# Optimization experiments

Hardware: AMD Instinct MI355X
Metric: run time of the kernel (lower is better)

## Reference

```python
import jax, jax.numpy as jnp
import numpy as np

P1, P2, M1, M2, W_SEARCH, STEP = 7, 7, 18, 55, 37, 4
EPS = 1e-6  # F.pairwise_distance eps


def align_corners(x, s, value):
    N, C, H, W = x.shape
    i = (s - H % s + 1) % s
    j = (s - W % s + 1) % s
    x = jnp.pad(x, ((0, 0), (0, 0), (0, i), (0, j)), constant_values=value)
    rows = jnp.array([H - 1, H - 1 + i]); cols = jnp.arange(0, W - 1, s)
    sub = x[:, :, rows[:, None], cols[None, :]]
    x = x.at[:, :, rows[:, None], cols[None, :]].set(sub[:, :, ::-1, :])
    rws = jnp.arange(0, H - 1, s); cls = jnp.array([W - 1, W - 1 + j])
    sub = x[:, :, rws[:, None], cls[None, :]]
    x = x.at[:, :, rws[:, None], cls[None, :]].set(sub[:, :, :, ::-1])
    rr = jnp.array([H - 1, H - 1 + i]); cc = jnp.array([W - 1, W - 1 + j])
    sub = x[:, :, rr, cc]
    x = x.at[:, :, rr, cc].set(sub[:, :, ::-1])
    return x


def unfold(x, p):  # torch F.unfold ordering: (N, C*p*p, (H-p+1)*(W-p+1))
    N, C, H, W = x.shape
    Hp, Wp = H - p + 1, W - p + 1
    cols = jnp.stack([x[:, :, ki:ki + Hp, kj:kj + Wp] for ki in range(p) for kj in range(p)], axis=2)
    return cols.reshape(N, C * p * p, Hp * Wp)


def fold(cols, H, W, p, C):  # torch F.fold: overlap-add
    N = cols.shape[0]; Hp, Wp = H - p + 1, W - p + 1
    cols = cols.reshape(N, C, p, p, Hp, Wp)
    out = jnp.zeros((N, C, H, W), cols.dtype)
    for ki in range(p):
        for kj in range(p):
            out = out.at[:, :, ki:ki + Hp, kj:kj + Wp].add(cols[:, :, ki, kj])
    return out


def block_matching(x, m, p, w, s):
    v = w // 2
    N, C, H, W = x.shape
    patches = unfold(x, p).reshape(N, C * p * p, H - p + 1, W - p + 1)
    patches = align_corners(patches, s, jnp.inf)
    _, d, k, l = patches.shape
    ref = patches[:, :, ::s, ::s].transpose(0, 2, 3, 1)                # (N,K,L,d)
    pad = jnp.pad(patches, ((0, 0), (0, 0), (v, v), (v, v)), constant_values=jnp.inf).transpose(0, 2, 3, 1)
    K, L = ref.shape[1], ref.shape[2]
    col_idx = jnp.arange(w)[:, None] + s * jnp.arange(L)[None, :]      # (w,L)
    dists = []
    for i in range(w):  # fixed-size search-window loop (hyperparameter)
        pad_i = pad[:, i:i + k:s, :, :]                                # (N,K,l+2v,d)
        g = pad_i[:, :, col_idx, :]                                    # (N,K,w,L,d)
        diff = g - ref[:, :, None, :, :] + EPS
        dists.append(jnp.sqrt(jnp.sum(diff * diff, axis=-1)))         # (N,K,w,L)
    dist = jnp.stack(dists, axis=2)                                    # (N,K,wi,wj,L)
    dist = dist.transpose(0, 1, 4, 2, 3).reshape(N, K, L, w * w)
    dist = dist.at[:, :, :, v * w + v].set(-jnp.inf)                   # force self-match
    idx = jax.lax.top_k(-dist, m)[1]                                   # (N,K,L,m) smallest distances
    ind_row = idx // w - v
    ind_col = idx % w - v
    row_ref = align_corners(jnp.arange(H - p + 1).reshape(1, 1, -1, 1), s, 0)[0, 0, ::s, 0]
    col_ref = align_corners(jnp.arange(W - p + 1).reshape(1, 1, 1, -1), s, 0)[0, 0, 0, ::s]
    ir = jnp.minimum(row_ref[None, :, None, None] + ind_row, H - p)
    ic = jnp.minimum(col_ref[None, None, :, None] + ind_col, W - p)
    return (ir * (W - p + 1) + ic).reshape(N, -1)                      # (N, K*L*m), block-major then m


def group_patches(y, indices, m, p):
    N, C, H, W = y.shape
    n = C * p * p
    unf = unfold(y, p)
    g = jnp.take_along_axis(unf, jnp.broadcast_to(indices[:, None, :], (N, n, indices.shape[1])), axis=2)
    return g.transpose(0, 2, 1).reshape(N, -1, m, n)                   # (N,B,m,n)


def denoise1(Y, sigma):
    N, B, m, n = Y.shape
    YtY = jnp.einsum('nbik,nbjk->nbij', Y, Y)
    Lc = jnp.linalg.cholesky(YtY)
    rhs = YtY - n * sigma ** 2 * jnp.eye(m, dtype=Y.dtype)
    theta = jax.scipy.linalg.cho_solve((Lc, True), rhs)
    X_hat = jnp.einsum('nbij,nbjk->nbik', theta, Y)
    wts = 1.0 / jnp.clip(jnp.sum(theta ** 2, axis=3, keepdims=True), 1.0 / m, 1.0)
    return X_hat, wts


def denoise2(Y, X, sigma):
    N, B, m, n = Y.shape
    XtX = jnp.einsum('nbik,nbjk->nbij', X, X)
    Lc = jnp.linalg.cholesky(XtX + n * sigma ** 2 * jnp.eye(m, dtype=Y.dtype))
    theta = jax.scipy.linalg.cho_solve((Lc, True), XtX)
    X_hat = jnp.einsum('nbij,nbjk->nbik', theta, Y)
    wts = 1.0 / jnp.clip(jnp.sum(theta ** 2, axis=3, keepdims=True), 1.0 / m, 1.0)
    return X_hat, wts


def aggregation(X_hat, wts, indices, size, p):
    N, C, H, W = size
    n = C * p * p
    Ltot = (H - p + 1) * (W - p + 1)
    Xc = (X_hat * wts).transpose(0, 3, 1, 2).reshape(N, n, -1)         # (N,n,B*m)
    wc = jnp.broadcast_to(wts.reshape(N, 1, -1), Xc.shape)

    def scat(cols, idx):
        return jnp.zeros((n, Ltot), cols.dtype).at[:, idx].add(cols)

    Xs = jax.vmap(scat)(Xc, indices)
    Ws = jax.vmap(scat)(wc, indices)
    return fold(Xs, H, W, p, C) / fold(Ws, H, W, p, C)


def nlridge(input_y, sigma):
    # step 1: noisy self-similarity + ridge with known sigma
    y_mean = jnp.mean(input_y, axis=1, keepdims=True)
    idx1 = block_matching(jax.lax.stop_gradient(y_mean), M1, P1, W_SEARCH, STEP)
    Y1 = group_patches(input_y, idx1, M1, P1)
    X1, w1 = denoise1(Y1, sigma)
    den1 = aggregation(X1, w1, idx1, input_y.shape, P1)
    # step 2: pilot-guided matching + ridge
    x_mean = jnp.mean(den1, axis=1, keepdims=True)
    idx2 = block_matching(jax.lax.stop_gradient(x_mean), M2, P2, W_SEARCH, STEP)
    Y2 = group_patches(input_y, idx2, M2, P2)
    X2 = group_patches(den1, idx2, M2, P2)
    Xh, w2 = denoise2(Y2, X2, sigma)
    return aggregation(Xh, w2, idx2, input_y.shape, P2)


def setup_inputs() -> dict:
    key = jax.random.key(0)
    input_y = jax.random.uniform(key, (2, 1, 256, 256), dtype=jnp.float32)
    sigma = jnp.array([0.1], dtype=jnp.float32)  # ~25/255 noise level
    return {'input_y': input_y, 'sigma': sigma}


def reference(input_y, sigma):
    return nlridge(input_y, sigma)
```

## Files before the change

### kernel.cpp

```cpp
#include <hip/hip_runtime.h>
#include <math.h>

#define IMG_H 256
#define IMG_W 256
#define IMG_SZ (IMG_H * IMG_W)
#define NP 49
#define HP 250
#define NPAT 62500
#define NB 4096
#define NCAND 1369
#define VRAD 18
#define CENTER (VRAD * 37 + VRAD)
#define NIMG 2
#define YSTR 52
#define WSTR 55

__device__ __forceinline__ bool align_map(int r, int c, int& ro, int& co) {
    if (r < 0 || r > 252 || c < 0 || c > 252) return false;
    if (r == 252) {
        if (c == 252) { ro = 249; co = 249; return true; }
        if (c <= 248 && (c & 3) == 0) { ro = 249; co = c; return true; }
        return false;
    }
    if (c == 252) {
        if (r <= 248 && (r & 3) == 0) { ro = r; co = 249; return true; }
        return false;
    }
    if (r >= 250 || c >= 250) return false;
    if (r == 249) {
        if (c == 249) return false;
        if ((c & 3) == 0) return false;
        ro = 249; co = c; return true;
    }
    if (c == 249) {
        if ((r & 3) == 0) return false;
        ro = r; co = 249; return true;
    }
    ro = r; co = c; return true;
}

__global__ void zero_kernel(float* __restrict__ p, int total) {
    int i = blockIdx.x * blockDim.x + threadIdx.x;
    if (i < total) p[i] = 0.0f;
}

__global__ void div_kernel(const float* __restrict__ acc, float* __restrict__ out, int total) {
    int i = blockIdx.x * blockDim.x + threadIdx.x;
    if (i < total) out[i] = acc[2 * i] / acc[2 * i + 1];
}

__global__ __launch_bounds__(256) void fold_div_kernel(const float* __restrict__ Xacc,
                                                       const float* __restrict__ Wacc,
                                                       float* __restrict__ out) {
    int e = blockIdx.x * 256 + threadIdx.x;
    if (e >= NIMG * IMG_SZ) return;
    int n = e / IMG_SZ, pix = e % IMG_SZ;
    int r = pix / IMG_W, c = pix % IMG_W;
    const float* Xn = Xacc + (size_t)n * NPAT * NP;
    const float* Wn = Wacc + (size_t)n * NPAT;
    float num = 0.f, den = 0.f;
#pragma unroll
    for (int ki = 0; ki < 7; ++ki) {
        int pr = r - ki;
        if (pr < 0 || pr > HP - 1) continue;
#pragma unroll
        for (int kj = 0; kj < 7; ++kj) {
            int pc = c - kj;
            if (pc < 0 || pc > HP - 1) continue;
            int p = pr * HP + pc;
            num += Xn[(size_t)p * NP + ki * 7 + kj];
            den += Wn[p];
        }
    }
    out[e] = num / den;
}

template <int M>
__global__ __launch_bounds__(256) void bm_kernel(const float* __restrict__ img,
                                                 int* __restrict__ idx_out) {
    __shared__ float win[43 * WSTR];
    __shared__ float dist[4][NCAND];
    const int llb = blockIdx.x, kk = blockIdx.y, n = blockIdx.z;
    const float* im = img + (size_t)n * IMG_SZ;
    const int t = threadIdx.x;
    const int w = t >> 6, lane = t & 63;
    const int ll = 4 * llb + w;
    const int rr = (kk < 63) ? 4 * kk : 249;
    const int cc = (ll < 63) ? 4 * ll : 249;
    const int ar0 = 4 * kk, ac0 = 4 * ll;
    const int acb = 16 * llb;
    const int row0 = max(0, ar0 - VRAD), col0 = max(0, acb - VRAD);
    const int row1 = min(IMG_H - 1, ar0 + VRAD + 6);
    const int col1 = min(IMG_W - 1, acb + 12 + VRAD + 6);
    const int nr = row1 - row0 + 1, nc = col1 - col0 + 1;
    for (int e = t; e < nr * nc; e += 256) {
        int r = e / nc, c = e % nc;
        win[r * WSTR + c] = im[(row0 + r) * IMG_W + col0 + c];
    }
    __syncthreads();
    float rf[NP];
    {
        const float* rb = &win[(rr - row0) * WSTR + (cc - col0)];
#pragma unroll
        for (int ki = 0; ki < 7; ++ki)
#pragma unroll
            for (int kj = 0; kj < 7; ++kj) rf[ki * 7 + kj] = rb[ki * WSTR + kj];
    }
    float* dw = dist[w];
    for (int cand = lane; cand < NCAND; cand += 64) {
        const int dr = cand / 37 - VRAD, dc = cand % 37 - VRAD;
        int ro, co;
        float d;
        if (align_map(ar0 + dr, ac0 + dc, ro, co)) {
            const float* base = &win[(ro - row0) * WSTR + (co - col0)];
            float s = 0.f;
#pragma unroll
            for (int ki = 0; ki < 7; ++ki)
#pragma unroll
                for (int kj = 0; kj < 7; ++kj) {
                    float df = base[ki * WSTR + kj] - rf[ki * 7 + kj] + 1e-6f;
                    s = fmaf(df, df, s);
                }
            d = sqrtf(s);
        } else {
            d = INFINITY;
        }
        if (cand == CENTER) d = -1.0f;
        dw[cand] = d;
    }
    __syncthreads();
    float v1 = INFINITY, v2 = INFINITY;
    int i1 = NCAND, i2 = NCAND;
    for (int c = lane; c < NCAND; c += 64) {
        float v = dw[c];
        if (v < v1) { v2 = v1; i2 = i1; v1 = v; i1 = c; }
        else if (v < v2) { v2 = v; i2 = c; }
    }
    int* out = idx_out + (size_t)((n * 64 + kk) * 64 + ll) * M;
    for (int sel = 0; sel < M; ++sel) {
        float gv = v1;
        int gi = i1;
#pragma unroll
        for (int off = 32; off; off >>= 1) {
            float vv = __shfl_xor(gv, off);
            int ii = __shfl_xor(gi, off);
            if (vv < gv || (vv == gv && ii < gi)) { gv = vv; gi = ii; }
        }
        if (lane == 0) {
            int dr = gi / 37 - VRAD, dc = gi % 37 - VRAD;
            out[sel] = min(rr + dr, 249) * HP + min(cc + dc, 249);
        }
        if ((gi & 63) == lane) {
            dw[gi] = INFINITY;
            v1 = v2; i1 = i2; v2 = INFINITY; i2 = NCAND;
            if (i1 == NCAND) {
                for (int c = lane; c < NCAND; c += 64) {
                    float v = dw[c];
                    if (v < v1) { v2 = v1; i2 = i1; v1 = v; i1 = c; }
                    else if (v < v2) { v2 = v; i2 = c; }
                }
            }
        }
    }
}

template <int M, bool R2, bool AGGP>
__global__ __launch_bounds__(128, 2) void denoise_kernel(
    const float* __restrict__ y, const float* __restrict__ xsrc,
    const int* __restrict__ idx, const float* __restrict__ sigma_p,
    float* __restrict__ accPix, float* __restrict__ Xacc, float* __restrict__ Wacc) {
    constexpr int PADM = (M + 3) & ~3;
    constexpr int NCH = PADM / 4;
    constexpr int TPK = M * (M + 1) / 2;
    constexpr int NS = (TPK + 127) / 128;
    struct RO { static constexpr int f(int i) {
        int a = i >> 2, b = i & 3; return 8 * a * (a + 1) + 4 * (a + 1) * b; } };
    constexpr int LSZ = RO::f(PADM);
    constexpr int YOFF = LSZ;
    constexpr int UN = LSZ + M * YSTR;
    __shared__ __align__(16) float SU[UN];
    __shared__ float cbuf[64];
    __shared__ __align__(16) float rdiag[PADM];
    __shared__ float wsh[M];
    __shared__ int gix[M];
    const int b = blockIdx.x, n = blockIdx.y;
    const int t = threadIdx.x;
    const int lane = t & 63, wv = t >> 6;
    if (t < M) gix[t] = idx[(size_t)(n * NB + b) * M + t];
    __syncthreads();
    const float* im = y + (size_t)n * IMG_SZ;
    const float* xim = xsrc + (size_t)n * IMG_SZ;
    {
        const float* src = R2 ? xim : im;
        float* dst = R2 ? &SU[0] : &SU[YOFF];
        for (int e = t; e < M * YSTR; e += 128) {
            int i = e / YSTR, ch = e - i * YSTR;
            float v = 0.f;
            if (ch < NP) {
                int p = gix[i];
                v = src[(p / HP + ch / 7) * IMG_W + (p % HP + ch % 7)];
            }
            dst[i * YSTR + ch] = v;
        }
    }
    __syncthreads();
    const float sg = sigma_p[0];
    const float cns = 49.f * sg * sg;
    int siR[NS], sjR[NS];
    float gsum[NS];
#pragma unroll
    for (int s = 0; s < NS; ++s) {
        int e = t + 128 * s;
        if (e < TPK) {
            int i = (int)((sqrtf(8.f * e + 1.f) - 1.f) * 0.5f);
            while ((i + 1) * (i + 2) / 2 <= e) ++i;
            while (i * (i + 1) / 2 > e) --i;
            siR[s] = i;
            sjR[s] = e - i * (i + 1) / 2;
        } else {
            siR[s] = -1;
            sjR[s] = 0;
        }
    }
    {
        const float* base = R2 ? &SU[0] : &SU[YOFF];
#pragma unroll
        for (int s = 0; s < NS; ++s) {
            float sum = 0.f;
            if (siR[s] >= 0) {
                const float* Pi = base + siR[s] * YSTR;
                const float* Pj = base + sjR[s] * YSTR;
#pragma unroll
                for (int q = 0; q < 13; ++q) {
                    float4 a = *(const float4*)(Pi + 4 * q);
                    float4 c4 = *(const float4*)(Pj + 4 * q);
                    sum = fmaf(a.x, c4.x, sum);
                    sum = fmaf(a.y, c4.y, sum);
                    sum = fmaf(a.z, c4.z, sum);
                    sum = fmaf(a.w, c4.w, sum);
                }
                if (R2 && siR[s] == sjR[s]) sum += cns;
            }
            gsum[s] = sum;
        }
    }
    __syncthreads();
#pragma unroll
    for (int s = 0; s < NS; ++s)
        if (siR[s] >= 0) SU[RO::f(siR[s]) + sjR[s]] = gsum[s];
    if (R2) {
        for (int e = t; e < M * YSTR; e += 128) {
            int i = e / YSTR, ch = e - i * YSTR;
            float v = 0.f;
            if (ch < NP) {
                int p = gix[i];
                v = im[(p / HP + ch / 7) * IMG_W + (p % HP + ch % 7)];
            }
            SU[YOFF + i * YSTR + ch] = v;
        }
    }
    __syncthreads();
    if (wv == 0) {
        float g[PADM];
        if (lane < M) {
#pragma unroll
            for (int j = 0; j < PADM; ++j) {
                if (j >= M) g[j] = 0.f;
                else g[j] = (j <= lane) ? SU[RO::f(lane) + j] : SU[RO::f(j) + lane];
            }
        } else {
#pragma unroll
            for (int j = 0; j < PADM; ++j) g[j] = (j == lane) ? 1.f : 0.f;
        }
#pragma unroll
        for (int k = 0; k < PADM - 1; ++k) {
            cbuf[lane] = g[k];
            float ivd = 1.f / cbuf[k];
            float fk = g[k] * ivd;
#pragma unroll
            for (int jb = (k + 1) / 4; jb < NCH; ++jb) {
                float4 cv = *(const float4*)&cbuf[4 * jb];
                if (4 * jb + 0 > k) g[4 * jb + 0] = fmaf(-fk, cv.x, g[4 * jb + 0]);
                if (4 * jb + 1 > k) g[4 * jb + 1] = fmaf(-fk, cv.y, g[4 * jb + 1]);
                if (4 * jb + 2 > k) g[4 * jb + 2] = fmaf(-fk, cv.z, g[4 * jb + 2]);
                if (4 * jb + 3 > k) g[4 * jb + 3] = fmaf(-fk, cv.w, g[4 * jb + 3]);
            }
        }
        if (lane < PADM) rdiag[lane] = (lane < M) ? 1.f / sqrtf(g[lane]) : 1.f;
        if (lane < PADM) {
#pragma unroll
            for (int jb = 0; jb < NCH; ++jb) {
                if (4 * jb <= lane) {
                    float4 rd4 = *(const float4*)&rdiag[4 * jb];
                    float4 o;
                    o.x = g[4 * jb + 0] * rd4.x;
                    o.y = g[4 * jb + 1] * rd4.y;
                    o.z = g[4 * jb + 2] * rd4.z;
                    o.w = g[4 * jb + 3] * rd4.w;
                    *(float4*)&SU[RO::f(lane) + 4 * jb] = o;
                }
            }
        }
    }
    __syncthreads();
    const bool isId = (wv == 0) && (lane < M);
    const bool isY = (wv == 1) && (lane < NP);
    const int ch = (wv == 1 && lane < NP) ? lane : 0;
    float bb[PADM];
    if (wv == 1) {
#pragma unroll
        for (int i = 0; i < PADM; ++i) bb[i] = (i < M) ? SU[YOFF + i * YSTR + ch] : 0.f;
    } else {
#pragma unroll
        for (int i = 0; i < PADM; ++i) bb[i] = (i == lane) ? 1.f : 0.f;
    }
#pragma unroll
    for (int ck = 0; ck < NCH; ++ck) {
        const int i0 = 4 * ck;
        float L10 = SU[RO::f(4 * ck + 1) + 4 * ck];
        float L20 = SU[RO::f(4 * ck + 2) + 4 * ck], L21 = SU[RO::f(4 * ck + 2) + 4 * ck + 1];
        float L30 = SU[RO::f(4 * ck + 3) + 4 * ck], L31 = SU[RO::f(4 * ck + 3) + 4 * ck + 1],
              L32 = SU[RO::f(4 * ck + 3) + 4 * ck + 2];
        float b0 = bb[i0] * rdiag[i0];
        float b1 = (bb[i0 + 1] - L10 * b0) * rdiag[i0 + 1];
        float b2 = (bb[i0 + 2] - L20 * b0 - L21 * b1) * rdiag[i0 + 2];
        float b3 = (bb[i0 + 3] - L30 * b0 - L31 * b1 - L32 * b2) * rdiag[i0 + 3];
        bb[i0] = b0; bb[i0 + 1] = b1; bb[i0 + 2] = b2; bb[i0 + 3] = b3;
#pragma unroll
        for (int j = 4 * ck + 4; j < PADM; ++j) {
            float4 L4 = *(const float4*)&SU[RO::f(j) + 4 * ck];
            bb[j] = fmaf(-L4.x, b0, fmaf(-L4.y, b1, fmaf(-L4.z, b2, fmaf(-L4.w, b3, bb[j]))));
        }
        if (ck & 1) asm volatile("" ::: "memory");
    }
#pragma unroll
    for (int i = PADM - 1; i >= 0; --i) {
        float bbi = bb[i] * rdiag[i];
        bb[i] = bbi;
#pragma unroll
        for (int qb = 0; qb < i / 4; ++qb) {
            float4 L4 = *(const float4*)&SU[RO::f(i) + 4 * qb];
            bb[4 * qb + 0] = fmaf(-L4.x, bbi, bb[4 * qb + 0]);
            bb[4 * qb + 1] = fmaf(-L4.y, bbi, bb[4 * qb + 1]);
            bb[4 * qb + 2] = fmaf(-L4.z, bbi, bb[4 * qb + 2]);
            bb[4 * qb + 3] = fmaf(-L4.w, bbi, bb[4 * qb + 3]);
        }
#pragma unroll
        for (int j = i & ~3; j < i; ++j)
            bb[j] = fmaf(-SU[RO::f(i) + j], bbi, bb[j]);
        if ((i & 7) == 0) asm volatile("" ::: "memory");
    }
    float wloc = 0.f;
    if (isId) {
        float s2 = 0.f;
#pragma unroll
        for (int i = 0; i < M; ++i) {
            float th = ((i == lane) ? 1.f : 0.f) - cns * bb[i];
            s2 = fmaf(th, th, s2);
        }
        s2 = fminf(fmaxf(s2, 1.f / (float)M), 1.f);
        wloc = 1.f / s2;
        wsh[lane] = wloc;
    }
    if (!AGGP && isY) {
#pragma unroll
        for (int i = 0; i < M; ++i)
            SU[YOFF + i * YSTR + ch] = fmaf(-cns, bb[i], SU[YOFF + i * YSTR + ch]);
    }
    __syncthreads();
    if (AGGP) {
        if (isId) atomicAdd(&Wacc[(size_t)n * NPAT + gix[lane]], wloc);
        if (isY) {
#pragma unroll
            for (int i = 0; i < M; ++i) {
                float xv = fmaf(-cns, bb[i], SU[YOFF + i * YSTR + ch]);
                atomicAdd(&Xacc[((size_t)n * NPAT + gix[i]) * NP + ch], xv * wsh[i]);
            }
        }
    } else {
        float* aA = accPix + (size_t)n * IMG_SZ * 2;
        for (int e = t; e < M * NP; e += 128) {
            int i = e / NP, c2 = e % NP;
            int p = gix[i];
            int pix = (p / HP + c2 / 7) * IMG_W + (p % HP + c2 % 7);
            float wi = wsh[i];
            atomicAdd(&aA[pix * 2], SU[YOFF + i * YSTR + c2] * wi);
            atomicAdd(&aA[pix * 2 + 1], wi);
        }
    }
}

extern "C" void kernel_launch(void* const* d_in, const int* in_sizes, int n_in,
                              void* d_out, int out_size, void* d_ws, size_t ws_size,
                              hipStream_t stream) {
    const float* y = (const float*)d_in[0];
    const float* sigma = (const float*)d_in[1];
    float* out = (float*)d_out;

    char* ws = (char*)d_ws;
    size_t off = 0;
    auto carve = [&](size_t bytes) {
        void* p = ws + off;
        off += (bytes + 255) & ~(size_t)255;
        return p;
    };
    int* idx1 = (int*)carve((size_t)NIMG * NB * 18 * sizeof(int));
    int* idx2 = (int*)carve((size_t)NIMG * NB * 55 * sizeof(int));
    float* accPix = (float*)carve((size_t)NIMG * IMG_SZ * 2 * sizeof(float));
    float* den1 = (float*)carve((size_t)NIMG * IMG_SZ * sizeof(float));
    const size_t xw_floats = (size_t)NIMG * NPAT * (NP + 1);
    float* Xacc = (float*)carve(xw_floats * sizeof(float));
    float* Wacc = Xacc + (size_t)NIMG * NPAT * NP;
    const bool patchMode = (off <= ws_size);

    const int imgTotal = NIMG * IMG_SZ;

    if (patchMode) {
        const int xwTotal = (int)xw_floats;
        zero_kernel<<<(xwTotal + 255) / 256, 256, 0, stream>>>(Xacc, xwTotal);
        bm_kernel<18><<<dim3(16, 64, NIMG), 256, 0, stream>>>(y, idx1);
        denoise_kernel<18, false, true><<<dim3(NB, NIMG), 128, 0, stream>>>(
            y, y, idx1, sigma, accPix, Xacc, Wacc);
        fold_div_kernel<<<(imgTotal + 255) / 256, 256, 0, stream>>>(Xacc, Wacc, den1);
        zero_kernel<<<(xwTotal + 255) / 256, 256, 0, stream>>>(Xacc, xwTotal);
        bm_kernel<55><<<dim3(16, 64, NIMG), 256, 0, stream>>>(den1, idx2);
        denoise_kernel<55, true, true><<<dim3(NB, NIMG), 128, 0, stream>>>(
            y, den1, idx2, sigma, accPix, Xacc, Wacc);
        fold_div_kernel<<<(imgTotal + 255) / 256, 256, 0, stream>>>(Xacc, Wacc, out);
    } else {
        const int accTotal = NIMG * IMG_SZ * 2;
        zero_kernel<<<(accTotal + 255) / 256, 256, 0, stream>>>(accPix, accTotal);
        bm_kernel<18><<<dim3(16, 64, NIMG), 256, 0, stream>>>(y, idx1);
        denoise_kernel<18, false, false><<<dim3(NB, NIMG), 128, 0, stream>>>(
            y, y, idx1, sigma, accPix, Xacc, Wacc);
        div_kernel<<<(imgTotal + 255) / 256, 256, 0, stream>>>(accPix, den1, imgTotal);
        zero_kernel<<<(accTotal + 255) / 256, 256, 0, stream>>>(accPix, accTotal);
        bm_kernel<55><<<dim3(16, 64, NIMG), 256, 0, stream>>>(den1, idx2);
        denoise_kernel<55, true, false><<<dim3(NB, NIMG), 128, 0, stream>>>(
            y, den1, idx2, sigma, accPix, Xacc, Wacc);
        div_kernel<<<(imgTotal + 255) / 256, 256, 0, stream>>>(accPix, out, imgTotal);
    }
}
```

Measured before the change: 960.6 us.

## Aggregate denoised patches in shared-memory pixel tiles before global atomics

```diff
diff --git a/kernel.cpp b/kernel.cpp
--- a/kernel.cpp
+++ b/kernel.cpp
@@ -6,7 +6,6 @@
 #define IMG_SZ (IMG_H * IMG_W)
 #define NP 49
 #define HP 250
-#define NPAT 62500
 #define NB 4096
 #define NCAND 1369
 #define VRAD 18
@@ -14,6 +13,8 @@
 #define NIMG 2
 #define YSTR 52
 #define WSTR 55
+#define PXR 43
+#define PXC 56
 
 __device__ __forceinline__ bool align_map(int r, int c, int& ro, int& co) {
     if (r < 0 || r > 252 || c < 0 || c > 252) return false;
@@ -47,32 +48,6 @@
 __global__ void div_kernel(const float* __restrict__ acc, float* __restrict__ out, int total) {
     int i = blockIdx.x * blockDim.x + threadIdx.x;
     if (i < total) out[i] = acc[2 * i] / acc[2 * i + 1];
-}
-
-__global__ __launch_bounds__(256) void fold_div_kernel(const float* __restrict__ Xacc,
-                                                       const float* __restrict__ Wacc,
-                                                       float* __restrict__ out) {
-    int e = blockIdx.x * 256 + threadIdx.x;
-    if (e >= NIMG * IMG_SZ) return;
-    int n = e / IMG_SZ, pix = e % IMG_SZ;
-    int r = pix / IMG_W, c = pix % IMG_W;
-    const float* Xn = Xacc + (size_t)n * NPAT * NP;
-    const float* Wn = Wacc + (size_t)n * NPAT;
-    float num = 0.f, den = 0.f;
-#pragma unroll
-    for (int ki = 0; ki < 7; ++ki) {
-        int pr = r - ki;
-        if (pr < 0 || pr > HP - 1) continue;
-#pragma unroll
-        for (int kj = 0; kj < 7; ++kj) {
-            int pc = c - kj;
-            if (pc < 0 || pc > HP - 1) continue;
-            int p = pr * HP + pc;
-            num += Xn[(size_t)p * NP + ki * 7 + kj];
-            den += Wn[p];
-        }
-    }
-    out[e] = num / den;
 }
 
 template <int M>
@@ -164,11 +139,11 @@
     }
 }
 
-template <int M, bool R2, bool AGGP>
+template <int M, bool R2>
 __global__ __launch_bounds__(128, 2) void denoise_kernel(
     const float* __restrict__ y, const float* __restrict__ xsrc,
     const int* __restrict__ idx, const float* __restrict__ sigma_p,
-    float* __restrict__ accPix, float* __restrict__ Xacc, float* __restrict__ Wacc) {
+    float* __restrict__ accPix) {
     constexpr int PADM = (M + 3) & ~3;
     constexpr int NCH = PADM / 4;
     constexpr int TPK = M * (M + 1) / 2;
@@ -179,35 +154,24 @@
     constexpr int YOFF = LSZ;
     constexpr int UN = LSZ + M * YSTR;
     __shared__ __align__(16) float SU[UN];
+    __shared__ float Nl[PXR * PXC];
+    __shared__ float Wl[PXR * PXC];
     __shared__ float cbuf[64];
     __shared__ __align__(16) float rdiag[PADM];
     __shared__ float wsh[M];
     __shared__ int gix[M];
-    const int b = blockIdx.x, n = blockIdx.y;
+    const int llb = blockIdx.x, kk = blockIdx.y, n = blockIdx.z;
     const int t = threadIdx.x;
     const int lane = t & 63, wv = t >> 6;
-    if (t < M) gix[t] = idx[(size_t)(n * NB + b) * M + t];
-    __syncthreads();
+    const int rrRef = (kk < 63) ? 4 * kk : 249;
+    const int row0p = max(0, rrRef - VRAD);
+    const int col0p = max(0, 16 * llb - VRAD);
     const float* im = y + (size_t)n * IMG_SZ;
     const float* xim = xsrc + (size_t)n * IMG_SZ;
-    {
-        const float* src = R2 ? xim : im;
-        float* dst = R2 ? &SU[0] : &SU[YOFF];
-        for (int e = t; e < M * YSTR; e += 128) {
-            int i = e / YSTR, ch = e - i * YSTR;
-            float v = 0.f;
-            if (ch < NP) {
-                int p = gix[i];
-                v = src[(p / HP + ch / 7) * IMG_W + (p % HP + ch % 7)];
-            }
-            dst[i * YSTR + ch] = v;
-        }
-    }
-    __syncthreads();
     const float sg = sigma_p[0];
     const float cns = 49.f * sg * sg;
+    for (int e = t; e < PXR * PXC; e += 128) { Nl[e] = 0.f; Wl[e] = 0.f; }
     int siR[NS], sjR[NS];
-    float gsum[NS];
 #pragma unroll
     for (int s = 0; s < NS; ++s) {
         int e = t + 128 * s;
@@ -222,170 +186,190 @@
             sjR[s] = 0;
         }
     }
-    {
-        const float* base = R2 ? &SU[0] : &SU[YOFF];
-#pragma unroll
-        for (int s = 0; s < NS; ++s) {
-            float sum = 0.f;
-            if (siR[s] >= 0) {
-                const float* Pi = base + siR[s] * YSTR;
-                const float* Pj = base + sjR[s] * YSTR;
-#pragma unroll
-                for (int q = 0; q < 13; ++q) {
-                    float4 a = *(const float4*)(Pi + 4 * q);
-                    float4 c4 = *(const float4*)(Pj + 4 * q);
-                    sum = fmaf(a.x, c4.x, sum);
-                    sum = fmaf(a.y, c4.y, sum);
-                    sum = fmaf(a.z, c4.z, sum);
-                    sum = fmaf(a.w, c4.w, sum);
-                }
-                if (R2 && siR[s] == sjR[s]) sum += cns;
-            }
-            gsum[s] = sum;
-        }
-    }
-    __syncthreads();
-#pragma unroll
-    for (int s = 0; s < NS; ++s)
-        if (siR[s] >= 0) SU[RO::f(siR[s]) + sjR[s]] = gsum[s];
-    if (R2) {
-        for (int e = t; e < M * YSTR; e += 128) {
-            int i = e / YSTR, ch = e - i * YSTR;
-            float v = 0.f;
-            if (ch < NP) {
-                int p = gix[i];
-                v = im[(p / HP + ch / 7) * IMG_W + (p % HP + ch % 7)];
-            }
-            SU[YOFF + i * YSTR + ch] = v;
-        }
-    }
-    __syncthreads();
-    if (wv == 0) {
-        float g[PADM];
-        if (lane < M) {
-#pragma unroll
-            for (int j = 0; j < PADM; ++j) {
-                if (j >= M) g[j] = 0.f;
-                else g[j] = (j <= lane) ? SU[RO::f(lane) + j] : SU[RO::f(j) + lane];
-            }
+#pragma unroll 1
+    for (int g = 0; g < 4; ++g) {
+        __syncthreads();
+        if (t < M) gix[t] = idx[(size_t)(n * NB + kk * 64 + 4 * llb + g) * M + t];
+        __syncthreads();
+        {
+            const float* src = R2 ? xim : im;
+            float* dst = R2 ? &SU[0] : &SU[YOFF];
+            for (int e = t; e < M * YSTR; e += 128) {
+                int i = e / YSTR, ch = e - i * YSTR;
+                float v = 0.f;
+                if (ch < NP) {
+                    int p = gix[i];
+                    v = src[(p / HP + ch / 7) * IMG_W + (p % HP + ch % 7)];
+                }
+                dst[i * YSTR + ch] = v;
+            }
+        }
+        __syncthreads();
+        float gsum[NS];
+        {
+            const float* base = R2 ? &SU[0] : &SU[YOFF];
+#pragma unroll
+            for (int s = 0; s < NS; ++s) {
+                float sum = 0.f;
+                if (siR[s] >= 0) {
+                    const float* Pi = base + siR[s] * YSTR;
+                    const float* Pj = base + sjR[s] * YSTR;
+#pragma unroll
+                    for (int q = 0; q < 13; ++q) {
+                        float4 a = *(const float4*)(Pi + 4 * q);
+                        float4 c4 = *(const float4*)(Pj + 4 * q);
+                        sum = fmaf(a.x, c4.x, sum);
+                        sum = fmaf(a.y, c4.y, sum);
+                        sum = fmaf(a.z, c4.z, sum);
+                        sum = fmaf(a.w, c4.w, sum);
+                    }
+                    if (R2 && siR[s] == sjR[s]) sum += cns;
+                }
+                gsum[s] = sum;
+            }
+        }
+        __syncthreads();
+#pragma unroll
+        for (int s = 0; s < NS; ++s)
+            if (siR[s] >= 0) SU[RO::f(siR[s]) + sjR[s]] = gsum[s];
+        if (R2) {
+            for (int e = t; e < M * YSTR; e += 128) {
+                int i = e / YSTR, ch = e - i * YSTR;
+                float v = 0.f;
+                if (ch < NP) {
+                    int p = gix[i];
+                    v = im[(p / HP + ch / 7) * IMG_W + (p % HP + ch % 7)];
+                }
+                SU[YOFF + i * YSTR + ch] = v;
+            }
+        }
+        __syncthreads();
+        if (wv == 0) {
+            float gr_[PADM];
+            if (lane < M) {
+#pragma unroll
+                for (int j = 0; j < PADM; ++j) {
+                    if (j >= M) gr_[j] = 0.f;
+                    else gr_[j] = (j <= lane) ? SU[RO::f(lane) + j] : SU[RO::f(j) + lane];
+                }
+            } else {
+#pragma unroll
+                for (int j = 0; j < PADM; ++j) gr_[j] = (j == lane) ? 1.f : 0.f;
+            }
+#pragma unroll
+            for (int k = 0; k < PADM - 1; ++k) {
+                cbuf[lane] = gr_[k];
+                float ivd = 1.f / cbuf[k];
+                float fk = gr_[k] * ivd;
+#pragma unroll
+                for (int jb = (k + 1) / 4; jb < NCH; ++jb) {
+                    float4 cv = *(const float4*)&cbuf[4 * jb];
+                    if (4 * jb + 0 > k) gr_[4 * jb + 0] = fmaf(-fk, cv.x, gr_[4 * jb + 0]);
+                    if (4 * jb + 1 > k) gr_[4 * jb + 1] = fmaf(-fk, cv.y, gr_[4 * jb + 1]);
+                    if (4 * jb + 2 > k) gr_[4 * jb + 2] = fmaf(-fk, cv.z, gr_[4 * jb + 2]);
+                    if (4 * jb + 3 > k) gr_[4 * jb + 3] = fmaf(-fk, cv.w, gr_[4 * jb + 3]);
+                }
+            }
+            if (lane < PADM) rdiag[lane] = (lane < M) ? 1.f / sqrtf(gr_[lane]) : 1.f;
+            if (lane < PADM) {
+#pragma unroll
+                for (int jb = 0; jb < NCH; ++jb) {
+                    if (4 * jb <= lane) {
+                        float4 rd4 = *(const float4*)&rdiag[4 * jb];
+                        float4 o;
+                        o.x = gr_[4 * jb + 0] * rd4.x;
+                        o.y = gr_[4 * jb + 1] * rd4.y;
+                        o.z = gr_[4 * jb + 2] * rd4.z;
+                        o.w = gr_[4 * jb + 3] * rd4.w;
+                        *(float4*)&SU[RO::f(lane) + 4 * jb] = o;
+                    }
+                }
+            }
+        }
+        __syncthreads();
+        const bool isId = (wv == 0) && (lane < M);
+        const bool isY = (wv == 1) && (lane < NP);
+        const int ch = (wv == 1 && lane < NP) ? lane : 0;
+        float bb[PADM];
+        if (wv == 1) {
+#pragma unroll
+            for (int i = 0; i < PADM; ++i) bb[i] = (i < M) ? SU[YOFF + i * YSTR + ch] : 0.f;
         } else {
 #pragma unroll
-            for (int j = 0; j < PADM; ++j) g[j] = (j == lane) ? 1.f : 0.f;
-        }
-#pragma unroll
-        for (int k = 0; k < PADM - 1; ++k) {
-            cbuf[lane] = g[k];
-            float ivd = 1.f / cbuf[k];
-            float fk = g[k] * ivd;
-#pragma unroll
-            for (int jb = (k + 1) / 4; jb < NCH; ++jb) {
-                float4 cv = *(const float4*)&cbuf[4 * jb];
-                if (4 * jb + 0 > k) g[4 * jb + 0] = fmaf(-fk, cv.x, g[4 * jb + 0]);
-                if (4 * jb + 1 > k) g[4 * jb + 1] = fmaf(-fk, cv.y, g[4 * jb + 1]);
-                if (4 * jb + 2 > k) g[4 * jb + 2] = fmaf(-fk, cv.z, g[4 * jb + 2]);
-                if (4 * jb + 3 > k) g[4 * jb + 3] = fmaf(-fk, cv.w, g[4 * jb + 3]);
-            }
-        }
-        if (lane < PADM) rdiag[lane] = (lane < M) ? 1.f / sqrtf(g[lane]) : 1.f;
-        if (lane < PADM) {
-#pragma unroll
-            for (int jb = 0; jb < NCH; ++jb) {
-                if (4 * jb <= lane) {
-                    float4 rd4 = *(const float4*)&rdiag[4 * jb];
-                    float4 o;
-                    o.x = g[4 * jb + 0] * rd4.x;
-                    o.y = g[4 * jb + 1] * rd4.y;
-                    o.z = g[4 * jb + 2] * rd4.z;
-                    o.w = g[4 * jb + 3] * rd4.w;
-                    *(float4*)&SU[RO::f(lane) + 4 * jb] = o;
-                }
-            }
-        }
-    }
-    __syncthreads();
-    const bool isId = (wv == 0) && (lane < M);
-    const bool isY = (wv == 1) && (lane < NP);
-    const int ch = (wv == 1 && lane < NP) ? lane : 0;
-    float bb[PADM];
-    if (wv == 1) {
-#pragma unroll
-        for (int i = 0; i < PADM; ++i) bb[i] = (i < M) ? SU[YOFF + i * YSTR + ch] : 0.f;
-    } else {
-#pragma unroll
-        for (int i = 0; i < PADM; ++i) bb[i] = (i == lane) ? 1.f : 0.f;
-    }
-#pragma unroll
-    for (int ck = 0; ck < NCH; ++ck) {
-        const int i0 = 4 * ck;
-        float L10 = SU[RO::f(4 * ck + 1) + 4 * ck];
-        float L20 = SU[RO::f(4 * ck + 2) + 4 * ck], L21 = SU[RO::f(4 * ck + 2) + 4 * ck + 1];
-        float L30 = SU[RO::f(4 * ck + 3) + 4 * ck], L31 = SU[RO::f(4 * ck + 3) + 4 * ck + 1],
-              L32 = SU[RO::f(4 * ck + 3) + 4 * ck + 2];
-        float b0 = bb[i0] * rdiag[i0];
-        float b1 = (bb[i0 + 1] - L10 * b0) * rdiag[i0 + 1];
-        float b2 = (bb[i0 + 2] - L20 * b0 - L21 * b1) * rdiag[i0 + 2];
-        float b3 = (bb[i0 + 3] - L30 * b0 - L31 * b1 - L32 * b2) * rdiag[i0 + 3];
-        bb[i0] = b0; bb[i0 + 1] = b1; bb[i0 + 2] = b2; bb[i0 + 3] = b3;
-#pragma unroll
-        for (int j = 4 * ck + 4; j < PADM; ++j) {
-            float4 L4 = *(const float4*)&SU[RO::f(j) + 4 * ck];
-            bb[j] = fmaf(-L4.x, b0, fmaf(-L4.y, b1, fmaf(-L4.z, b2, fmaf(-L4.w, b3, bb[j]))));
-        }
-        if (ck & 1) asm volatile("" ::: "memory");
-    }
-#pragma unroll
-    for (int i = PADM - 1; i >= 0; --i) {
-        float bbi = bb[i] * rdiag[i];
-        bb[i] = bbi;
-#pragma unroll
-        for (int qb = 0; qb < i / 4; ++qb) {
-            float4 L4 = *(const float4*)&SU[RO::f(i) + 4 * qb];
-            bb[4 * qb + 0] = fmaf(-L4.x, bbi, bb[4 * qb + 0]);
-            bb[4 * qb + 1] = fmaf(-L4.y, bbi, bb[4 * qb + 1]);
-            bb[4 * qb + 2] = fmaf(-L4.z, bbi, bb[4 * qb + 2]);
-            bb[4 * qb + 3] = fmaf(-L4.w, bbi, bb[4 * qb + 3]);
-        }
-#pragma unroll
-        for (int j = i & ~3; j < i; ++j)
-            bb[j] = fmaf(-SU[RO::f(i) + j], bbi, bb[j]);
-        if ((i & 7) == 0) asm volatile("" ::: "memory");
-    }
-    float wloc = 0.f;
-    if (isId) {
-        float s2 = 0.f;
-#pragma unroll
-        for (int i = 0; i < M; ++i) {
-            float th = ((i == lane) ? 1.f : 0.f) - cns * bb[i];
-            s2 = fmaf(th, th, s2);
-        }
-        s2 = fminf(fmaxf(s2, 1.f / (float)M), 1.f);
-        wloc = 1.f / s2;
-        wsh[lane] = wloc;
-    }
-    if (!AGGP && isY) {
-#pragma unroll
-        for (int i = 0; i < M; ++i)
-            SU[YOFF + i * YSTR + ch] = fmaf(-cns, bb[i], SU[YOFF + i * YSTR + ch]);
-    }
-    __syncthreads();
-    if (AGGP) {
-        if (isId) atomicAdd(&Wacc[(size_t)n * NPAT + gix[lane]], wloc);
+            for (int i = 0; i < PADM; ++i) bb[i] = (i == lane) ? 1.f : 0.f;
+        }
+#pragma unroll
+        for (int ck = 0; ck < NCH; ++ck) {
+            const int i0 = 4 * ck;
+            float L10 = SU[RO::f(4 * ck + 1) + 4 * ck];
+            float L20 = SU[RO::f(4 * ck + 2) + 4 * ck], L21 = SU[RO::f(4 * ck + 2) + 4 * ck + 1];
+            float L30 = SU[RO::f(4 * ck + 3) + 4 * ck], L31 = SU[RO::f(4 * ck + 3) + 4 * ck + 1],
+                  L32 = SU[RO::f(4 * ck + 3) + 4 * ck + 2];
+            float b0 = bb[i0] * rdiag[i0];
+            float b1 = (bb[i0 + 1] - L10 * b0) * rdiag[i0 + 1];
+            float b2 = (bb[i0 + 2] - L20 * b0 - L21 * b1) * rdiag[i0 + 2];
+            float b3 = (bb[i0 + 3] - L30 * b0 - L31 * b1 - L32 * b2) * rdiag[i0 + 3];
+            bb[i0] = b0; bb[i0 + 1] = b1; bb[i0 + 2] = b2; bb[i0 + 3] = b3;
+#pragma unroll
+            for (int j = 4 * ck + 4; j < PADM; ++j) {
+                float4 L4 = *(const float4*)&SU[RO::f(j) + 4 * ck];
+                bb[j] = fmaf(-L4.x, b0, fmaf(-L4.y, b1, fmaf(-L4.z, b2, fmaf(-L4.w, b3, bb[j]))));
+            }
+            if (ck & 1) asm volatile("" ::: "memory");
+        }
+#pragma unroll
+        for (int i = PADM - 1; i >= 0; --i) {
+            float bbi = bb[i] * rdiag[i];
+            bb[i] = bbi;
+#pragma unroll
+            for (int qb = 0; qb < i / 4; ++qb) {
+                float4 L4 = *(const float4*)&SU[RO::f(i) + 4 * qb];
+                bb[4 * qb + 0] = fmaf(-L4.x, bbi, bb[4 * qb + 0]);
+                bb[4 * qb + 1] = fmaf(-L4.y, bbi, bb[4 * qb + 1]);
+                bb[4 * qb + 2] = fmaf(-L4.z, bbi, bb[4 * qb + 2]);
+                bb[4 * qb + 3] = fmaf(-L4.w, bbi, bb[4 * qb + 3]);
+            }
+#pragma unroll
+            for (int j = i & ~3; j < i; ++j)
+                bb[j] = fmaf(-SU[RO::f(i) + j], bbi, bb[j]);
+            if ((i & 7) == 0) asm volatile("" ::: "memory");
+        }
+        if (isId) {
+            float s2 = 0.f;
+#pragma unroll
+            for (int i = 0; i < M; ++i) {
+                float th = ((i == lane) ? 1.f : 0.f) - cns * bb[i];
+                s2 = fmaf(th, th, s2);
+            }
+            s2 = fminf(fmaxf(s2, 1.f / (float)M), 1.f);
+            wsh[lane] = 1.f / s2;
+        }
         if (isY) {
 #pragma unroll
-            for (int i = 0; i < M; ++i) {
-                float xv = fmaf(-cns, bb[i], SU[YOFF + i * YSTR + ch]);
-                atomicAdd(&Xacc[((size_t)n * NPAT + gix[i]) * NP + ch], xv * wsh[i]);
-            }
-        }
-    } else {
-        float* aA = accPix + (size_t)n * IMG_SZ * 2;
+            for (int i = 0; i < M; ++i)
+                SU[YOFF + i * YSTR + ch] = fmaf(-cns, bb[i], SU[YOFF + i * YSTR + ch]);
+        }
+        __syncthreads();
         for (int e = t; e < M * NP; e += 128) {
             int i = e / NP, c2 = e % NP;
             int p = gix[i];
-            int pix = (p / HP + c2 / 7) * IMG_W + (p % HP + c2 % 7);
+            int lr = (p / HP + c2 / 7) - row0p;
+            int lc = (p % HP + c2 % 7) - col0p;
             float wi = wsh[i];
-            atomicAdd(&aA[pix * 2], SU[YOFF + i * YSTR + c2] * wi);
-            atomicAdd(&aA[pix * 2 + 1], wi);
+            atomicAdd(&Nl[lr * PXC + lc], SU[YOFF + i * YSTR + c2] * wi);
+            atomicAdd(&Wl[lr * PXC + lc], wi);
+        }
+    }
+    __syncthreads();
+    float* aA = accPix + (size_t)n * IMG_SZ * 2;
+    for (int e = t; e < PXR * PXC; e += 128) {
+        float w = Wl[e];
+        if (w != 0.f) {
+            int gr2 = row0p + e / PXC, gc = col0p + e % PXC;
+            if (gr2 < IMG_H && gc < IMG_W) {
+                atomicAdd(&aA[(gr2 * IMG_W + gc) * 2], Nl[e]);
+                atomicAdd(&aA[(gr2 * IMG_W + gc) * 2 + 1], w);
+            }
         }
     }
 }
@@ -408,36 +392,17 @@
     int* idx2 = (int*)carve((size_t)NIMG * NB * 55 * sizeof(int));
     float* accPix = (float*)carve((size_t)NIMG * IMG_SZ * 2 * sizeof(float));
     float* den1 = (float*)carve((size_t)NIMG * IMG_SZ * sizeof(float));
-    const size_t xw_floats = (size_t)NIMG * NPAT * (NP + 1);
-    float* Xacc = (float*)carve(xw_floats * sizeof(float));
-    float* Wacc = Xacc + (size_t)NIMG * NPAT * NP;
-    const bool patchMode = (off <= ws_size);
-
+
+    const int accTotal = NIMG * IMG_SZ * 2;
     const int imgTotal = NIMG * IMG_SZ;
 
-    if (patchMode) {
-        const int xwTotal = (int)xw_floats;
-        zero_kernel<<<(xwTotal + 255) / 256, 256, 0, stream>>>(Xacc, xwTotal);
-        bm_kernel<18><<<dim3(16, 64, NIMG), 256, 0, stream>>>(y, idx1);
-        denoise_kernel<18, false, true><<<dim3(NB, NIMG), 128, 0, stream>>>(
-            y, y, idx1, sigma, accPix, Xacc, Wacc);
-        fold_div_kernel<<<(imgTotal + 255) / 256, 256, 0, stream>>>(Xacc, Wacc, den1);
-        zero_kernel<<<(xwTotal + 255) / 256, 256, 0, stream>>>(Xacc, xwTotal);
-        bm_kernel<55><<<dim3(16, 64, NIMG), 256, 0, stream>>>(den1, idx2);
-        denoise_kernel<55, true, true><<<dim3(NB, NIMG), 128, 0, stream>>>(
-            y, den1, idx2, sigma, accPix, Xacc, Wacc);
-        fold_div_kernel<<<(imgTotal + 255) / 256, 256, 0, stream>>>(Xacc, Wacc, out);
-    } else {
-        const int accTotal = NIMG * IMG_SZ * 2;
-        zero_kernel<<<(accTotal + 255) / 256, 256, 0, stream>>>(accPix, accTotal);
-        bm_kernel<18><<<dim3(16, 64, NIMG), 256, 0, stream>>>(y, idx1);
-        denoise_kernel<18, false, false><<<dim3(NB, NIMG), 128, 0, stream>>>(
-            y, y, idx1, sigma, accPix, Xacc, Wacc);
-        div_kernel<<<(imgTotal + 255) / 256, 256, 0, stream>>>(accPix, den1, imgTotal);
-        zero_kernel<<<(accTotal + 255) / 256, 256, 0, stream>>>(accPix, accTotal);
-        bm_kernel<55><<<dim3(16, 64, NIMG), 256, 0, stream>>>(den1, idx2);
-        denoise_kernel<55, true, false><<<dim3(NB, NIMG), 128, 0, stream>>>(
-            y, den1, idx2, sigma, accPix, Xacc, Wacc);
-        div_kernel<<<(imgTotal + 255) / 256, 256, 0, stream>>>(accPix, out, imgTotal);
-    }
-}
+    zero_kernel<<<(accTotal + 255) / 256, 256, 0, stream>>>(accPix, accTotal);
+    bm_kernel<18><<<dim3(16, 64, NIMG), 256, 0, stream>>>(y, idx1);
+    denoise_kernel<18, false><<<dim3(16, 64, NIMG), 128, 0, stream>>>(y, y, idx1, sigma, accPix);
+    div_kernel<<<(imgTotal + 255) / 256, 256, 0, stream>>>(accPix, den1, imgTotal);
+
+    zero_kernel<<<(accTotal + 255) / 256, 256, 0, stream>>>(accPix, accTotal);
+    bm_kernel<55><<<dim3(16, 64, NIMG), 256, 0, stream>>>(den1, idx2);
+    denoise_kernel<55, true><<<dim3(16, 64, NIMG), 128, 0, stream>>>(y, den1, idx2, sigma, accPix);
+    div_kernel<<<(imgTotal + 255) / 256, 256, 0, stream>>>(accPix, out, imgTotal);
+}
```

After: 1.565 ms. 1.63x slower.
